# Kernel tuning notes

Measured on AMD Instinct MI355X. Metric: run time of the kernel, lower is better.

The kernel has to match this reference:

```python
import jax, jax.numpy as jnp
import numpy as np

GN_EPS = 1e-5
GN_GROUPS = 8
KNN_EPS = 1e-8


def group_norm(x, w, b):
    # x: [B, C, N]
    B, C, N = x.shape
    xg = x.reshape(B, GN_GROUPS, C // GN_GROUPS, N)
    mu = jnp.mean(xg, axis=(2, 3), keepdims=True)
    var = jnp.var(xg, axis=(2, 3), keepdims=True)
    xg = (xg - mu) * jax.lax.rsqrt(var + GN_EPS)
    return xg.reshape(B, C, N) * w[None, :, None] + b[None, :, None]


def swish(x):
    return x * jax.nn.sigmoid(x)


def three_interpolate(points_coords, centers_coords, centers_features):
    # points_coords [B,3,N], centers_coords [B,3,M], centers_features [B,C,M]
    B, _, N = points_coords.shape
    C = centers_features.shape[1]
    p2 = jnp.sum(points_coords ** 2, axis=1)            # [B,N]
    c2 = jnp.sum(centers_coords ** 2, axis=1)           # [B,M]
    cross = jnp.einsum('bdn,bdm->bnm', points_coords, centers_coords)
    dist2 = p2[:, :, None] + c2[:, None, :] - 2.0 * cross  # [B,N,M] squared dists
    neg_d, idx = jax.lax.top_k(-dist2, 3)               # 3 smallest -> [B,N,3]
    d = -neg_d
    w = 1.0 / (d + KNN_EPS)
    w = w / jnp.sum(w, axis=-1, keepdims=True)          # [B,N,3]
    featsT = jnp.swapaxes(centers_features, 1, 2)       # [B,M,C]
    gathered = jnp.take_along_axis(featsT, idx.reshape(B, N * 3, 1), axis=1)
    gathered = gathered.reshape(B, N, 3, C)
    out = jnp.einsum('bnk,bnkc->bcn', w, gathered)      # [B,C,N]
    return out


def setup_inputs() -> dict:
    key = jax.random.key(0)
    ks = jax.random.split(key, 8)
    B, N, M = 8, 8192, 2048
    C_ctr, C_pts, D = 256, 128, 64
    Cin, C1, C2 = C_ctr + C_pts, 256, 256
    return {
        'points_coords': jax.random.normal(ks[0], (B, 3, N), jnp.float32),
        'centers_coords': jax.random.normal(ks[1], (B, 3, M), jnp.float32),
        'centers_features': jax.random.normal(ks[2], (B, C_ctr, M), jnp.float32),
        'points_features': jax.random.normal(ks[3], (B, C_pts, N), jnp.float32),
        'time_emb': jax.random.normal(ks[4], (B, D, 1), jnp.float32),
        'W1': jax.random.normal(ks[5], (C1, Cin), jnp.float32) * (1.0 / np.sqrt(Cin)),
        'b1': jnp.zeros((C1,), jnp.float32),
        'gn1_w': jnp.ones((C1,), jnp.float32),
        'gn1_b': jnp.zeros((C1,), jnp.float32),
        'W2': jax.random.normal(ks[6], (C2, C1), jnp.float32) * (1.0 / np.sqrt(C1)),
        'b2': jnp.zeros((C2,), jnp.float32),
        'gn2_w': jnp.ones((C2,), jnp.float32),
        'gn2_b': jnp.zeros((C2,), jnp.float32),
    }


def reference(points_coords, centers_coords, centers_features, points_features,
              time_emb, W1, b1, gn1_w, gn1_b, W2, b2, gn2_w, gn2_b):
    interp = three_interpolate(points_coords, centers_coords, centers_features)
    x = jnp.concatenate([interp, points_features], axis=1)  # [B, Cin, N]
    # SharedMLP layer 1: Conv1d(k=1) + GroupNorm(8) + Swish
    x = jnp.einsum('oc,bcn->bon', W1, x) + b1[None, :, None]
    x = swish(group_norm(x, gn1_w, gn1_b))
    # layer 2
    x = jnp.einsum('oc,bcn->bon', W2, x) + b2[None, :, None]
    x = swish(group_norm(x, gn2_w, gn2_b))
    N = points_coords.shape[-1]
    time_emb_exp = jnp.broadcast_to(time_emb[:, :, 0:1], time_emb.shape[:2] + (N,))
    return (x, points_coords, time_emb_exp)
```

## Files before the change

kernel.cpp:

```cpp
#include <hip/hip_runtime.h>
#include <hip/hip_bf16.h>
#include <float.h>

#define B_ 8
#define N_ 8192
#define M_ 2048
#define CC_ 256
#define CP_ 128
#define CIN_ 384
#define GRP_ 8
#define BN_ (B_ * N_)

typedef __attribute__((ext_vector_type(8))) short short8;
typedef __attribute__((ext_vector_type(4))) short short4v;
typedef __attribute__((ext_vector_type(4))) float f32x4;

static __device__ __forceinline__ float bf2f(unsigned short u) {
  union { unsigned int i; float f; } v; v.i = ((unsigned int)u) << 16; return v.f;
}
static __device__ __forceinline__ unsigned short f2bf(float f) {
  union { float f; unsigned int i; } v; v.f = f;
  unsigned int u = v.i;
  unsigned int r = (u + 0x7FFFu + ((u >> 16) & 1u)) >> 16;
  return (unsigned short)r;
}
static __device__ __forceinline__ void gload16(const void* g, void* l) {
  __builtin_amdgcn_global_load_lds(
      (const __attribute__((address_space(1))) void*)g,
      (__attribute__((address_space(3))) void*)l, 16, 0, 0);
}

__global__ __launch_bounds__(512) void k_front(
    const float* __restrict__ pc, const float* __restrict__ cc,
    int* __restrict__ idx, float* __restrict__ wts,
    const float* __restrict__ W1, const float* __restrict__ W2,
    short* __restrict__ W1b, short* __restrict__ W2b,
    const float* __restrict__ cf, short* __restrict__ FT,
    const float* __restrict__ pf, short* __restrict__ x0T,
    const float* __restrict__ te, float* __restrict__ out) {
  __shared__ __align__(16) char smem[32768];
  int bid = blockIdx.x;
  int t = threadIdx.x;
  if (bid < 512) {
    float4* ctr = (float4*)smem;
    double (*mk)[3][128] = (double(*)[3][128])smem;
    int b = bid >> 6;
    int base = (bid & 63) * 128;
    const float* ccb = cc + (size_t)b * 3 * M_;
    for (int i = t; i < M_; i += 512) {
      float x = ccb[i], y = ccb[M_ + i], z = ccb[2 * M_ + i];
      ctr[i] = make_float4(x, y, z, x * x + y * y + z * z);
    }
    __syncthreads();
    int wv = t >> 6, lane = t & 63;
    const float* pcb = pc + (size_t)b * 3 * N_;
    int na = base + lane, nb = base + 64 + lane;
    float pxa = pcb[na], pya = pcb[N_ + na], pza = pcb[2 * N_ + na];
    float pxb = pcb[nb], pyb = pcb[N_ + nb], pzb = pcb[2 * N_ + nb];
    float p2a = pxa * pxa + pya * pya + pza * pza;
    float p2b = pxb * pxb + pyb * pyb + pzb * pzb;
    const double kinit = __hiloint2double(0x7F7FFFFF, 0);
    double a0 = kinit, a1 = kinit, a2 = kinit;
    double e0 = kinit, e1 = kinit, e2 = kinit;
    const float4* C = ctr + wv * 256;
    int mbase = wv * 256;
#pragma unroll 8
    for (int m = 0; m < 256; ++m) {
      float4 c = C[m];
      float dota = pxa * c.x;
      dota = __builtin_fmaf(pya, c.y, dota);
      dota = __builtin_fmaf(pza, c.z, dota);
      float da = __builtin_fmaf(-2.f, dota, c.w) + p2a;
      float dotb = pxb * c.x;
      dotb = __builtin_fmaf(pyb, c.y, dotb);
      dotb = __builtin_fmaf(pzb, c.z, dotb);
      float db = __builtin_fmaf(-2.f, dotb, c.w) + p2b;
      double ka = __hiloint2double(__float_as_int(da), mbase + m);
      double kb = __hiloint2double(__float_as_int(db), mbase + m);
      double t0 = fmin(ka, a0);
      double t1 = fmin(fmax(ka, a0), a1);
      double t2 = fmin(fmax(ka, a1), a2);
      a0 = t0; a1 = t1; a2 = t2;
      double u0 = fmin(kb, e0);
      double u1 = fmin(fmax(kb, e0), e1);
      double u2 = fmin(fmax(kb, e1), e2);
      e0 = u0; e1 = u1; e2 = u2;
    }
    __syncthreads();
    mk[wv][0][lane] = a0; mk[wv][1][lane] = a1; mk[wv][2][lane] = a2;
    mk[wv][0][64 + lane] = e0; mk[wv][1][64 + lane] = e1; mk[wv][2][64 + lane] = e2;
    __syncthreads();
    if (t < 128) {
      double k0 = kinit, k1 = kinit, k2 = kinit;
#pragma unroll
      for (int w = 0; w < 8; ++w) {
#pragma unroll
        for (int j = 0; j < 3; ++j) {
          double key = mk[w][j][t];
          double n0 = fmin(key, k0);
          double n1 = fmin(fmax(key, k0), k1);
          double n2 = fmin(fmax(key, k1), k2);
          k0 = n0; k1 = n1; k2 = n2;
        }
      }
      float d0 = __int_as_float(__double2hiint(k0));
      float d1 = __int_as_float(__double2hiint(k1));
      float d2 = __int_as_float(__double2hiint(k2));
      float w0 = 1.f / (d0 + 1e-8f), w1 = 1.f / (d1 + 1e-8f), w2 = 1.f / (d2 + 1e-8f);
      float inv = 1.f / (w0 + w1 + w2);
      int bn = b * N_ + base + t;
      wts[bn] = w0 * inv; wts[BN_ + bn] = w1 * inv; wts[2 * BN_ + bn] = w2 * inv;
      idx[bn] = __double2loint(k0);
      idx[BN_ + bn] = __double2loint(k1);
      idx[2 * BN_ + bn] = __double2loint(k2);
    }
  } else if (bid < 704) {
    int i = (bid - 512) * 512 + t;
    if (i < 256 * CIN_) W1b[i] = (short)f2bf(W1[i]);
    if (i < 256 * 256)  W2b[i] = (short)f2bf(W2[i]);
  } else if (bid < 6848) {
    int q2 = (bid - 704) * 2 + (t >> 8);
    int tt = t & 255;
    float (*tile)[33] = (float(*)[33])(smem + (t >> 8) * 4352);
    const float* in; short* outp;
    int C, Nn, RS, coff, n0, c0, b;
    if (q2 < 4096) {
      in = cf; outp = FT; C = CC_; Nn = M_; RS = CC_; coff = 0;
      n0 = (q2 & 63) * 32; c0 = ((q2 >> 6) & 7) * 32; b = q2 >> 9;
    } else {
      int q = q2 - 4096;
      in = pf; outp = x0T; C = CP_; Nn = N_; RS = CIN_; coff = 256;
      n0 = (q & 255) * 32; c0 = ((q >> 8) & 3) * 32; b = q >> 10;
    }
    const float* inb = in + (size_t)b * C * Nn;
    short* outb = outp + (size_t)b * Nn * RS;
    int tx = tt & 31, ty = tt >> 5;
#pragma unroll
    for (int i = 0; i < 32; i += 8)
      tile[ty + i][tx] = inb[(size_t)(c0 + ty + i) * Nn + n0 + tx];
    __syncthreads();
#pragma unroll
    for (int i = 0; i < 32; i += 8)
      outb[(size_t)(n0 + ty + i) * RS + coff + c0 + tx] = (short)f2bf(tile[tx][ty + i]);
  } else {
    int total = 196608 + B_ * 64 * N_;
    for (int i = (bid - 6848) * 512 + t; i < total; i += 512 * 512) {
      if (i < 196608) {
        out[16777216 + i] = pc[i];
      } else {
        int j = i - 196608;
        int bd = j >> 13;
        out[16973824 + j] = te[bd];
      }
    }
  }
}

__global__ __launch_bounds__(256) void k_interp(
    const short* __restrict__ FT, const int* __restrict__ idx,
    const float* __restrict__ wts, short* __restrict__ x0T) {
  int b = blockIdx.y;
  int t = threadIdx.x;
  int nl = t >> 5, cch = (t & 31) * 8;
  int n = blockIdx.x * 8 + nl;
  int bn = b * N_ + n;
  int i0 = idx[bn], i1 = idx[BN_ + bn], i2 = idx[2 * BN_ + bn];
  float w0 = wts[bn], w1 = wts[BN_ + bn], w2 = wts[2 * BN_ + bn];
  const short* Fb = FT + (size_t)b * M_ * CC_;
  short8 f0 = *(const short8*)(Fb + (size_t)i0 * CC_ + cch);
  short8 f1 = *(const short8*)(Fb + (size_t)i1 * CC_ + cch);
  short8 f2 = *(const short8*)(Fb + (size_t)i2 * CC_ + cch);
  short8 r;
#pragma unroll
  for (int e = 0; e < 8; ++e) {
    float v = w0 * bf2f((unsigned short)f0[e]) + w1 * bf2f((unsigned short)f1[e]) +
              w2 * bf2f((unsigned short)f2[e]);
    r[e] = (short)f2bf(v);
  }
  *(short8*)(x0T + (size_t)bn * CIN_ + cch) = r;
}

template <int GNX>
__global__ __launch_bounds__(512) void k_gemm(
    const short* __restrict__ Wb, const short* __restrict__ Xb,
    const float* __restrict__ bias, short* __restrict__ Yb,
    float* __restrict__ part, int K,
    const float* __restrict__ partX, const float* __restrict__ gwX,
    const float* __restrict__ gbX) {
  __shared__ __align__(16) short sW[256 * 64];
  __shared__ __align__(16) short sX[128 * 64];
  __shared__ float4 fs2[256];
  __shared__ float fsm[16];
  int b = blockIdx.z;
  int ntile = blockIdx.y * 128;
  int t = threadIdx.x;
  int wv = t >> 6, lane = t & 63;
  int wr = wv >> 2, wc = wv & 3;
  int fr = lane & 15;
  int g = lane >> 4;
  if constexpr (GNX) {
    if (t < 8) {
      float s = 0.f, ss = 0.f;
      for (int j = 0; j < 64; ++j) {
        s += partX[(((size_t)b * 8 + t) * 64 + j) * 2];
        ss += partX[(((size_t)b * 8 + t) * 64 + j) * 2 + 1];
      }
      const float cnt = 32.f * 8192.f;
      float mean = s / cnt;
      float var = ss / cnt - mean * mean;
      fsm[t * 2] = mean;
      fsm[t * 2 + 1] = rsqrtf(var + 1e-5f);
    }
    __syncthreads();
    if (t < 256) {
      int gg = t >> 5;
      fs2[t] = make_float4(fsm[gg * 2], fsm[gg * 2 + 1], gwX[t], gbX[t]);
    }
    __syncthreads();
  }
  f32x4 acc[4][4] = {};
  const short* Wp = Wb;
  const short* Xp = Xb + ((size_t)b * N_ + ntile) * K;
  for (int k0 = 0; k0 < K; k0 += 64) {
#pragma unroll
    for (int j = 0; j < 4; ++j) {
      int s = j * 512 + t;
      int row = s >> 3;
      int kc = (s & 7) ^ (row & 7);
      gload16(Wp + (size_t)row * K + k0 + kc * 8, sW + j * 4096 + wv * 512);
    }
    if constexpr (!GNX) {
#pragma unroll
      for (int j = 0; j < 2; ++j) {
        int s = j * 512 + t;
        int row = s >> 3;
        int kc = (s & 7) ^ (row & 7);
        gload16(Xp + (size_t)row * K + k0 + kc * 8, sX + j * 4096 + wv * 512);
      }
    } else {
      int s0 = t, s1 = 512 + t;
      int row0 = s0 >> 3, sc0 = s0 & 7, kc0 = sc0 ^ (row0 & 7);
      int row1 = s1 >> 3, sc1 = s1 & 7, kc1 = sc1 ^ (row1 & 7);
      short8 v0 = *(const short8*)(Xp + (size_t)row0 * K + k0 + kc0 * 8);
      short8 v1 = *(const short8*)(Xp + (size_t)row1 * K + k0 + kc1 * 8);
      int o0 = k0 + kc0 * 8, o1 = k0 + kc1 * 8;
      short8 r0, r1;
#pragma unroll
      for (int e = 0; e < 8; ++e) {
        float4 p = fs2[o0 + e];
        float a = bf2f((unsigned short)v0[e]);
        a = (a - p.x) * p.y * p.z + p.w;
        a = a / (1.f + __expf(-a));
        r0[e] = (short)f2bf(a);
      }
#pragma unroll
      for (int e = 0; e < 8; ++e) {
        float4 p = fs2[o1 + e];
        float a = bf2f((unsigned short)v1[e]);
        a = (a - p.x) * p.y * p.z + p.w;
        a = a / (1.f + __expf(-a));
        r1[e] = (short)f2bf(a);
      }
      *(short8*)(sX + row0 * 64 + sc0 * 8) = r0;
      *(short8*)(sX + row1 * 64 + sc1 * 8) = r1;
    }
    __syncthreads();
#pragma unroll
    for (int h = 0; h < 2; ++h) {
      short8 af[4], bfr[4];
#pragma unroll
      for (int m = 0; m < 4; ++m) {
        int ra = wc * 64 + m * 16 + fr;
        af[m] = *(const short8*)(sW + ra * 64 + (((h * 4 + g) ^ (ra & 7)) << 3));
        int rb = wr * 64 + m * 16 + fr;
        bfr[m] = *(const short8*)(sX + rb * 64 + (((h * 4 + g) ^ (rb & 7)) << 3));
      }
#pragma unroll
      for (int m = 0; m < 4; ++m)
#pragma unroll
        for (int nn = 0; nn < 4; ++nn)
          acc[m][nn] = __builtin_amdgcn_mfma_f32_16x16x32_bf16(af[m], bfr[nn], acc[m][nn], 0, 0, 0);
    }
    __syncthreads();
  }
  float s01 = 0.f, ss01 = 0.f, s23 = 0.f, ss23 = 0.f;
#pragma unroll
  for (int m = 0; m < 4; ++m) {
    int o = wc * 64 + m * 16 + g * 4;
    float4 bi = *(const float4*)(bias + o);
#pragma unroll
    for (int nn = 0; nn < 4; ++nn) {
      int n = ntile + wr * 64 + nn * 16 + fr;
      float v0 = acc[m][nn][0] + bi.x;
      float v1 = acc[m][nn][1] + bi.y;
      float v2 = acc[m][nn][2] + bi.z;
      float v3 = acc[m][nn][3] + bi.w;
      if (m < 2) { s01 += v0 + v1 + v2 + v3; ss01 += v0*v0 + v1*v1 + v2*v2 + v3*v3; }
      else       { s23 += v0 + v1 + v2 + v3; ss23 += v0*v0 + v1*v1 + v2*v2 + v3*v3; }
      short4v sv;
      sv[0] = (short)f2bf(v0);
      sv[1] = (short)f2bf(v1);
      sv[2] = (short)f2bf(v2);
      sv[3] = (short)f2bf(v3);
      *(short4v*)(Yb + ((size_t)b * N_ + n) * 256 + o) = sv;
    }
  }
#pragma unroll
  for (int off = 32; off > 0; off >>= 1) {
    s01 += __shfl_down(s01, off);
    ss01 += __shfl_down(ss01, off);
    s23 += __shfl_down(s23, off);
    ss23 += __shfl_down(ss23, off);
  }
  float* wred = (float*)sW;
  if (lane == 0) {
    wred[wv * 4 + 0] = s01; wred[wv * 4 + 1] = ss01;
    wred[wv * 4 + 2] = s23; wred[wv * 4 + 3] = ss23;
  }
  __syncthreads();
  if (t < 16) {
    int gl = t >> 1, sel = t & 1;
    int wcq = gl >> 1;
    int id = (gl & 1) * 2 + sel;
    float v = wred[(0 * 4 + wcq) * 4 + id] + wred[(1 * 4 + wcq) * 4 + id];
    part[(((size_t)b * 8 + gl) * 64 + blockIdx.y) * 2 + sel] = v;
  }
}

__global__ __launch_bounds__(256) void k_gnapply_out(
    const short* __restrict__ Y, const float* __restrict__ part,
    const float* __restrict__ gw, const float* __restrict__ gb,
    float* __restrict__ out) {
  __shared__ float tile[64][65];
  __shared__ float fs[16];
  int b = blockIdx.z;
  int t = threadIdx.x;
  if (t < 8) {
    float s = 0.f, ss = 0.f;
    for (int j = 0; j < 64; ++j) {
      s += part[(((size_t)b * 8 + t) * 64 + j) * 2];
      ss += part[(((size_t)b * 8 + t) * 64 + j) * 2 + 1];
    }
    const float cnt = 32.f * 8192.f;
    float mean = s / cnt;
    float var = ss / cnt - mean * mean;
    fs[t * 2] = mean;
    fs[t * 2 + 1] = rsqrtf(var + 1e-5f);
  }
  __syncthreads();
  int n0 = blockIdx.x * 64, o0 = blockIdx.y * 64;
  int row = t >> 5, dcol = t & 31;
  const unsigned int* Yd = (const unsigned int*)(Y + (size_t)b * N_ * 256);
  int o = o0 + dcol * 2;
  int g = o >> 5;
  float mean = fs[g * 2], rstd = fs[g * 2 + 1];
  float w0 = gw[o], w1 = gw[o + 1], bb0 = gb[o], bb1 = gb[o + 1];
#pragma unroll
  for (int p = 0; p < 8; ++p) {
    int n = n0 + p * 8 + row;
    unsigned int v = Yd[(size_t)n * 128 + (o0 >> 1) + dcol];
    float a = bf2f((unsigned short)(v & 0xFFFF));
    float c = bf2f((unsigned short)(v >> 16));
    a = (a - mean) * rstd * w0 + bb0; a = a / (1.f + __expf(-a));
    c = (c - mean) * rstd * w1 + bb1; c = c / (1.f + __expf(-c));
    tile[p * 8 + row][dcol * 2] = a;
    tile[p * 8 + row][dcol * 2 + 1] = c;
  }
  __syncthreads();
  int ol = t >> 2, nch = (t & 3) * 16;
  float* ob = out + ((size_t)(b * 256 + o0 + ol)) * N_ + n0 + nch;
#pragma unroll
  for (int c4 = 0; c4 < 16; c4 += 4) {
    float4 v4;
    v4.x = tile[nch + c4 + 0][ol];
    v4.y = tile[nch + c4 + 1][ol];
    v4.z = tile[nch + c4 + 2][ol];
    v4.w = tile[nch + c4 + 3][ol];
    *(float4*)(ob + c4) = v4;
  }
}

extern "C" void kernel_launch(void* const* d_in, const int* in_sizes, int n_in,
                              void* d_out, int out_size, void* d_ws, size_t ws_size,
                              hipStream_t stream) {
  const float* pc  = (const float*)d_in[0];
  const float* cc  = (const float*)d_in[1];
  const float* cf  = (const float*)d_in[2];
  const float* pf  = (const float*)d_in[3];
  const float* te  = (const float*)d_in[4];
  const float* W1  = (const float*)d_in[5];
  const float* b1  = (const float*)d_in[6];
  const float* g1w = (const float*)d_in[7];
  const float* g1b = (const float*)d_in[8];
  const float* W2  = (const float*)d_in[9];
  const float* b2  = (const float*)d_in[10];
  const float* g2w = (const float*)d_in[11];
  const float* g2b = (const float*)d_in[12];
  float* out = (float*)d_out;

  char* ws = (char*)d_ws;
  size_t off = 0;
  auto alloc = [&](size_t bytes) {
    char* p = ws + off;
    off += (bytes + 255) & ~(size_t)255;
    return p;
  };
  short* FT   = (short*)alloc((size_t)B_ * M_ * CC_ * 2);
  short* x0T  = (short*)alloc((size_t)B_ * N_ * CIN_ * 2);
  short* y1   = (short*)alloc((size_t)B_ * N_ * 256 * 2);
  short* W1b  = (short*)alloc(256 * 384 * 2);
  short* W2b  = (short*)alloc(256 * 256 * 2);
  int*   idx  = (int*)alloc((size_t)3 * BN_ * 4);
  float* wts  = (float*)alloc((size_t)3 * BN_ * 4);
  float* part1 = (float*)alloc(8 * 8 * 64 * 2 * 4);
  float* part2 = (float*)alloc(8 * 8 * 64 * 2 * 4);
  short* y2 = (short*)x0T;

  k_front<<<7360, 512, 0, stream>>>(pc, cc, idx, wts, W1, W2, W1b, W2b,
                                    cf, FT, pf, x0T, te, out);
  k_interp<<<dim3(N_ / 8, B_), 256, 0, stream>>>(FT, idx, wts, x0T);
  k_gemm<0><<<dim3(1, N_ / 128, B_), 512, 0, stream>>>(
      W1b, x0T, b1, y1, part1, CIN_, nullptr, nullptr, nullptr);
  k_gemm<1><<<dim3(1, N_ / 128, B_), 512, 0, stream>>>(
      W2b, y1, b2, y2, part2, 256, part1, g1w, g1b);
  k_gnapply_out<<<dim3(N_ / 64, 4, B_), 256, 0, stream>>>(y2, part2, g2w, g2b, out);
}
```

Measured before the change: 166.2 us.

## Fuse three-point interpolation gather into first GEMM's X tile load

Removes the separate interpolation kernel. The first GEMM now gathers the three neighbour feature rows for each point, weights them, and writes the result straight into shared memory for the first 256 K channels. The remaining point-feature channels still come from x0T. This removes a kernel launch and the write and re-read of the interpolated part of x0T. In exchange, the GEMM main loop now does scattered global loads and ALU work with no async load path. K also becomes a compile-time constant and the K loop is fully unrolled, which may raise register pressure.

```diff
diff --git a/kernel.cpp b/kernel.cpp
--- a/kernel.cpp
+++ b/kernel.cpp
@@ -156,37 +156,16 @@
   }
 }
 
-__global__ __launch_bounds__(256) void k_interp(
-    const short* __restrict__ FT, const int* __restrict__ idx,
-    const float* __restrict__ wts, short* __restrict__ x0T) {
-  int b = blockIdx.y;
-  int t = threadIdx.x;
-  int nl = t >> 5, cch = (t & 31) * 8;
-  int n = blockIdx.x * 8 + nl;
-  int bn = b * N_ + n;
-  int i0 = idx[bn], i1 = idx[BN_ + bn], i2 = idx[2 * BN_ + bn];
-  float w0 = wts[bn], w1 = wts[BN_ + bn], w2 = wts[2 * BN_ + bn];
-  const short* Fb = FT + (size_t)b * M_ * CC_;
-  short8 f0 = *(const short8*)(Fb + (size_t)i0 * CC_ + cch);
-  short8 f1 = *(const short8*)(Fb + (size_t)i1 * CC_ + cch);
-  short8 f2 = *(const short8*)(Fb + (size_t)i2 * CC_ + cch);
-  short8 r;
-#pragma unroll
-  for (int e = 0; e < 8; ++e) {
-    float v = w0 * bf2f((unsigned short)f0[e]) + w1 * bf2f((unsigned short)f1[e]) +
-              w2 * bf2f((unsigned short)f2[e]);
-    r[e] = (short)f2bf(v);
-  }
-  *(short8*)(x0T + (size_t)bn * CIN_ + cch) = r;
-}
-
-template <int GNX>
+template <int MODE>
 __global__ __launch_bounds__(512) void k_gemm(
     const short* __restrict__ Wb, const short* __restrict__ Xb,
     const float* __restrict__ bias, short* __restrict__ Yb,
-    float* __restrict__ part, int K,
+    float* __restrict__ part,
     const float* __restrict__ partX, const float* __restrict__ gwX,
-    const float* __restrict__ gbX) {
+    const float* __restrict__ gbX,
+    const short* __restrict__ FT, const int* __restrict__ idx,
+    const float* __restrict__ wts) {
+  constexpr int K = (MODE == 1) ? CIN_ : 256;
   __shared__ __align__(16) short sW[256 * 64];
   __shared__ __align__(16) short sX[128 * 64];
   __shared__ float4 fs2[256];
@@ -198,7 +177,7 @@
   int wr = wv >> 2, wc = wv & 3;
   int fr = lane & 15;
   int g = lane >> 4;
-  if constexpr (GNX) {
+  if constexpr (MODE == 2) {
     if (t < 8) {
       float s = 0.f, ss = 0.f;
       for (int j = 0; j < 64; ++j) {
@@ -218,9 +197,24 @@
     }
     __syncthreads();
   }
+  int r0 = t >> 3, r1 = 64 + (t >> 3);
+  int sc = t & 7;
+  int kc0 = sc ^ (r0 & 7), kc1 = sc ^ (r1 & 7);
+  int i0a, i1a, i2a, i0b, i1b, i2b;
+  float w0a, w1a, w2a, w0b, w1b_, w2b;
+  const short* Fb = nullptr;
+  if constexpr (MODE == 1) {
+    int bn0 = b * N_ + ntile + r0, bn1 = b * N_ + ntile + r1;
+    i0a = idx[bn0]; i1a = idx[BN_ + bn0]; i2a = idx[2 * BN_ + bn0];
+    w0a = wts[bn0]; w1a = wts[BN_ + bn0]; w2a = wts[2 * BN_ + bn0];
+    i0b = idx[bn1]; i1b = idx[BN_ + bn1]; i2b = idx[2 * BN_ + bn1];
+    w0b = wts[bn1]; w1b_ = wts[BN_ + bn1]; w2b = wts[2 * BN_ + bn1];
+    Fb = FT + (size_t)b * M_ * CC_;
+  }
   f32x4 acc[4][4] = {};
   const short* Wp = Wb;
   const short* Xp = Xb + ((size_t)b * N_ + ntile) * K;
+#pragma unroll
   for (int k0 = 0; k0 < K; k0 += 64) {
 #pragma unroll
     for (int j = 0; j < 4; ++j) {
@@ -229,29 +223,54 @@
       int kc = (s & 7) ^ (row & 7);
       gload16(Wp + (size_t)row * K + k0 + kc * 8, sW + j * 4096 + wv * 512);
     }
-    if constexpr (!GNX) {
-#pragma unroll
-      for (int j = 0; j < 2; ++j) {
-        int s = j * 512 + t;
-        int row = s >> 3;
-        int kc = (s & 7) ^ (row & 7);
-        gload16(Xp + (size_t)row * K + k0 + kc * 8, sX + j * 4096 + wv * 512);
+    if constexpr (MODE == 1) {
+      if (k0 < 256) {
+        int ch0 = k0 + kc0 * 8, ch1 = k0 + kc1 * 8;
+        short8 f0 = *(const short8*)(Fb + (size_t)i0a * CC_ + ch0);
+        short8 f1 = *(const short8*)(Fb + (size_t)i1a * CC_ + ch0);
+        short8 f2 = *(const short8*)(Fb + (size_t)i2a * CC_ + ch0);
+        short8 h0 = *(const short8*)(Fb + (size_t)i0b * CC_ + ch1);
+        short8 h1 = *(const short8*)(Fb + (size_t)i1b * CC_ + ch1);
+        short8 h2 = *(const short8*)(Fb + (size_t)i2b * CC_ + ch1);
+        short8 ra, rb;
+#pragma unroll
+        for (int e = 0; e < 8; ++e) {
+          float v = w0a * bf2f((unsigned short)f0[e]) + w1a * bf2f((unsigned short)f1[e]) +
+                    w2a * bf2f((unsigned short)f2[e]);
+          ra[e] = (short)f2bf(v);
+        }
+#pragma unroll
+        for (int e = 0; e < 8; ++e) {
+          float v = w0b * bf2f((unsigned short)h0[e]) + w1b_ * bf2f((unsigned short)h1[e]) +
+                    w2b * bf2f((unsigned short)h2[e]);
+          rb[e] = (short)f2bf(v);
+        }
+        *(short8*)(sX + r0 * 64 + sc * 8) = ra;
+        *(short8*)(sX + r1 * 64 + sc * 8) = rb;
+      } else {
+#pragma unroll
+        for (int j = 0; j < 2; ++j) {
+          int s = j * 512 + t;
+          int row = s >> 3;
+          int kc = (s & 7) ^ (row & 7);
+          gload16(Xp + (size_t)row * K + k0 + kc * 8, sX + j * 4096 + wv * 512);
+        }
       }
     } else {
       int s0 = t, s1 = 512 + t;
-      int row0 = s0 >> 3, sc0 = s0 & 7, kc0 = sc0 ^ (row0 & 7);
-      int row1 = s1 >> 3, sc1 = s1 & 7, kc1 = sc1 ^ (row1 & 7);
-      short8 v0 = *(const short8*)(Xp + (size_t)row0 * K + k0 + kc0 * 8);
-      short8 v1 = *(const short8*)(Xp + (size_t)row1 * K + k0 + kc1 * 8);
-      int o0 = k0 + kc0 * 8, o1 = k0 + kc1 * 8;
-      short8 r0, r1;
+      int row0 = s0 >> 3, sc0 = s0 & 7, kca = sc0 ^ (row0 & 7);
+      int row1 = s1 >> 3, sc1 = s1 & 7, kcb = sc1 ^ (row1 & 7);
+      short8 v0 = *(const short8*)(Xp + (size_t)row0 * K + k0 + kca * 8);
+      short8 v1 = *(const short8*)(Xp + (size_t)row1 * K + k0 + kcb * 8);
+      int o0 = k0 + kca * 8, o1 = k0 + kcb * 8;
+      short8 r0v, r1v;
 #pragma unroll
       for (int e = 0; e < 8; ++e) {
         float4 p = fs2[o0 + e];
         float a = bf2f((unsigned short)v0[e]);
         a = (a - p.x) * p.y * p.z + p.w;
         a = a / (1.f + __expf(-a));
-        r0[e] = (short)f2bf(a);
+        r0v[e] = (short)f2bf(a);
       }
 #pragma unroll
       for (int e = 0; e < 8; ++e) {
@@ -259,10 +278,10 @@
         float a = bf2f((unsigned short)v1[e]);
         a = (a - p.x) * p.y * p.z + p.w;
         a = a / (1.f + __expf(-a));
-        r1[e] = (short)f2bf(a);
-      }
-      *(short8*)(sX + row0 * 64 + sc0 * 8) = r0;
-      *(short8*)(sX + row1 * 64 + sc1 * 8) = r1;
+        r1v[e] = (short)f2bf(a);
+      }
+      *(short8*)(sX + row0 * 64 + sc0 * 8) = r0v;
+      *(short8*)(sX + row1 * 64 + sc1 * 8) = r1v;
     }
     __syncthreads();
 #pragma unroll
@@ -270,10 +289,10 @@
       short8 af[4], bfr[4];
 #pragma unroll
       for (int m = 0; m < 4; ++m) {
-        int ra = wc * 64 + m * 16 + fr;
-        af[m] = *(const short8*)(sW + ra * 64 + (((h * 4 + g) ^ (ra & 7)) << 3));
-        int rb = wr * 64 + m * 16 + fr;
-        bfr[m] = *(const short8*)(sX + rb * 64 + (((h * 4 + g) ^ (rb & 7)) << 3));
+        int ra_ = wc * 64 + m * 16 + fr;
+        af[m] = *(const short8*)(sW + ra_ * 64 + (((h * 4 + g) ^ (ra_ & 7)) << 3));
+        int rb_ = wr * 64 + m * 16 + fr;
+        bfr[m] = *(const short8*)(sX + rb_ * 64 + (((h * 4 + g) ^ (rb_ & 7)) << 3));
       }
 #pragma unroll
       for (int m = 0; m < 4; ++m)
@@ -418,10 +437,9 @@
 
   k_front<<<7360, 512, 0, stream>>>(pc, cc, idx, wts, W1, W2, W1b, W2b,
                                     cf, FT, pf, x0T, te, out);
-  k_interp<<<dim3(N_ / 8, B_), 256, 0, stream>>>(FT, idx, wts, x0T);
-  k_gemm<0><<<dim3(1, N_ / 128, B_), 512, 0, stream>>>(
-      W1b, x0T, b1, y1, part1, CIN_, nullptr, nullptr, nullptr);
   k_gemm<1><<<dim3(1, N_ / 128, B_), 512, 0, stream>>>(
-      W2b, y1, b2, y2, part2, 256, part1, g1w, g1b);
+      W1b, x0T, b1, y1, part1, nullptr, nullptr, nullptr, FT, idx, wts);
+  k_gemm<2><<<dim3(1, N_ / 128, B_), 512, 0, stream>>>(
+      W2b, y1, b2, y2, part2, part1, g1w, g1b, nullptr, nullptr, nullptr);
   k_gnapply_out<<<dim3(N_ / 64, 4, B_), 256, 0, stream>>>(y2, part2, g2w, g2b, out);
 }
```

Measured after the change: 168.3 us. About the same (+1.3%).
